# Kernel optimization log

Measured on AMD Instinct MI355X. Metric: run time of the kernel, lower is better.

The kernel has to match this reference:

```python
import jax, jax.numpy as jnp
import numpy as np

DIM = 384
H = W = 56
WS = 7
SS = 3
NH = 12
NMLP = 1536
N = WS * WS  # 49 tokens per window
EPS = 1e-5


def _rel_pos_index(ws):
    coords = np.stack(np.meshgrid(np.arange(ws), np.arange(ws), indexing='ij')).reshape(2, -1)
    rel = (coords[:, :, None] - coords[:, None, :]).transpose(1, 2, 0)
    rel[:, :, 0] += ws - 1
    rel[:, :, 1] += ws - 1
    rel[:, :, 0] *= 2 * ws - 1
    return rel.sum(-1)  # (N, N) int


def _attn_mask(Hh, Ww, ws, ss):
    img = np.zeros((Hh, Ww), dtype=np.float32)
    cnt = 0
    for h in (slice(0, -ws), slice(-ws, -ss), slice(-ss, None)):
        for w in (slice(0, -ws), slice(-ws, -ss), slice(-ss, None)):
            img[h, w] = cnt
            cnt += 1
    mw = img.reshape(Hh // ws, ws, Ww // ws, ws).transpose(0, 2, 1, 3).reshape(-1, ws * ws)
    diff = mw[:, None, :] - mw[:, :, None]  # (nW, N, N)
    return np.where(diff != 0, np.float32(-100.0), np.float32(0.0))


_REL_IDX = jnp.asarray(_rel_pos_index(WS))          # (49, 49)
_MASK = jnp.asarray(_attn_mask(H, W, WS, SS))       # (64, 49, 49)


def _ln(x, g, b):
    mu = jnp.mean(x, axis=-1, keepdims=True)
    var = jnp.mean(jnp.square(x - mu), axis=-1, keepdims=True)
    return (x - mu) * jax.lax.rsqrt(var + EPS) * g + b


def setup_inputs() -> dict:
    key = jax.random.key(0)
    ks = jax.random.split(key, 8)
    s = 0.02
    return {
        'x': jax.random.normal(ks[0], (32, H * W, DIM), dtype=jnp.float32),
        'g1': jnp.ones((DIM,), jnp.float32),
        'be1': jnp.zeros((DIM,), jnp.float32),
        'w_qkv': jax.random.normal(ks[1], (DIM, 3 * DIM), jnp.float32) * s,
        'b_qkv': jnp.zeros((3 * DIM,), jnp.float32),
        'rel_table': jax.random.normal(ks[2], ((2 * WS - 1) ** 2, NH), jnp.float32) * s,
        'w_proj': jax.random.normal(ks[3], (DIM, DIM), jnp.float32) * s,
        'b_proj': jnp.zeros((DIM,), jnp.float32),
        'g2': jnp.ones((DIM,), jnp.float32),
        'be2': jnp.zeros((DIM,), jnp.float32),
        'w1': jax.random.normal(ks[4], (DIM, NMLP), jnp.float32) * s,
        'b1': jnp.zeros((NMLP,), jnp.float32),
        'w2': jax.random.normal(ks[5], (NMLP, DIM), jnp.float32) * s,
        'b2': jnp.zeros((DIM,), jnp.float32),
    }


def reference(x, g1, be1, w_qkv, b_qkv, rel_table, w_proj, b_proj, g2, be2, w1, b1, w2, b2):
    B, L, C = x.shape
    hd = C // NH
    scale = hd ** -0.5

    shortcut = x
    h = _ln(x, g1, be1).reshape(B, H, W, C)
    h = jnp.roll(h, (-SS, -SS), axis=(1, 2))
    # window partition -> (B*nW, N, C)
    xw = h.reshape(B, H // WS, WS, W // WS, WS, C).transpose(0, 1, 3, 2, 4, 5).reshape(-1, N, C)
    B_ = xw.shape[0]

    qkv = (xw @ w_qkv + b_qkv).reshape(B_, N, 3, NH, hd).transpose(2, 0, 3, 1, 4)
    q, k, v = qkv[0], qkv[1], qkv[2]  # (B_, NH, N, hd)
    attn = jnp.einsum('whid,whjd->whij', q, k) * scale  # (B_, NH, N, N)

    bias = rel_table[_REL_IDX.reshape(-1)].reshape(N, N, NH).transpose(2, 0, 1)
    attn = attn + bias[None]

    nW = _MASK.shape[0]
    attn = attn.reshape(B_ // nW, nW, NH, N, N) + _MASK[None, :, None]
    attn = attn.reshape(B_, NH, N, N)
    attn = jax.nn.softmax(attn, axis=-1)

    out = jnp.einsum('whij,whjd->whid', attn, v).transpose(0, 2, 1, 3).reshape(B_, N, C)
    out = out @ w_proj + b_proj

    # window reverse -> (B, H, W, C)
    out = out.reshape(B, H // WS, W // WS, WS, WS, C).transpose(0, 1, 3, 2, 4, 5).reshape(B, H, W, C)
    out = jnp.roll(out, (SS, SS), axis=(1, 2)).reshape(B, L, C)

    x1 = out + shortcut
    m = _ln(x1, g2, be2)
    m = jax.nn.gelu(m @ w1 + b1, approximate=False) @ w2 + b2
    return m + x1
```

## Files before the change

kernel.cpp:

```cpp
#include <hip/hip_runtime.h>
#include <hip/hip_bf16.h>
#include <math.h>

typedef __attribute__((ext_vector_type(8))) short bf16x8;
typedef __attribute__((ext_vector_type(4))) short bf16x4;
typedef __attribute__((ext_vector_type(4))) float f32x4;
typedef __hip_bfloat16 bf16;

#define NH 12
#define HD 32
#define NPAD 64
#define NWIN 2048
#define NTOK 100352
#define HBLK (NPAD*HD)
#define WBLK (3*NH*HBLK)

typedef __attribute__((address_space(3))) const void cv3;

#define STR2(x) #x
#define DSR(dst, base, OFF)                                                  \
  asm volatile("ds_read_b128 %0, %1 offset:" STR2(OFF)                       \
               : "=v"(dst) : "v"(base))

__device__ inline float wave_sum(float v) {
#pragma unroll
  for (int off = 32; off; off >>= 1) v += __shfl_xor(v, off);
  return v;
}

__device__ inline void load_lds16(const bf16* g, bf16* l) {
  __builtin_amdgcn_global_load_lds((const __attribute__((address_space(1))) void*)g,
                                   (__attribute__((address_space(3))) void*)l, 16, 0, 0);
}

__device__ inline short bfbits(float f) {
  bf16 h = __float2bfloat16(f);
  return *(short*)&h;
}

__global__ __launch_bounds__(256) void cast_transpose(const float* __restrict__ in,
                                                      bf16* __restrict__ out, int K, int N) {
  int e = blockIdx.x * 256 + threadIdx.x;
  if (e >= K * N) return;
  int n = e / K, k = e - n * K;
  out[e] = __float2bfloat16(in[k * N + n]);
}

__global__ __launch_bounds__(256) void zero_pads(bf16* __restrict__ qkv) {
  int idx = blockIdx.x * 256 + threadIdx.x;
  const int total = NWIN * 3 * NH * 15 * HD;
  if (idx >= total) return;
  int d = idx & 31; int rest = idx >> 5;
  int n = 49 + (rest % 15); rest /= 15;
  int h = rest % NH; rest /= NH;
  int which = rest % 3; int w = rest / 3;
  size_t base = (size_t)w * WBLK + (size_t)which * NH * HBLK + (size_t)h * HBLK;
  size_t addr = (which == 2) ? base + (size_t)d * NPAD + n : base + (size_t)n * HD + d;
  qkv[addr] = __float2bfloat16(0.0f);
}

__global__ __launch_bounds__(256) void build_bias(const float* __restrict__ rel,
                                                  float* __restrict__ tbl) {
  int e = blockIdx.x * 256 + threadIdx.x;
  if (e >= 4 * 12 * 49 * 64) return;
  int col = e & 63; int t = e >> 6;
  int row = t % 49; t /= 49;
  int h = t % 12; int cls = t / 12;
  float v;
  if (col >= 49) {
    v = -1e30f;
  } else {
    int py = row / 7, px = row - py * 7;
    int qy = col / 7, qx = col - qy * 7;
    int ridx = (py - qy + 6) * 13 + (px - qx + 6);
    v = rel[ridx * 12 + h];
    int wy7 = cls >> 1, wx7 = cls & 1;
    int ly_r = wy7 ? (py < 4 ? 1 : 2) : 0;
    int lx_r = wx7 ? (px < 4 ? 1 : 2) : 0;
    int ly_c = wy7 ? (qy < 4 ? 1 : 2) : 0;
    int lx_c = wx7 ? (qx < 4 ? 1 : 2) : 0;
    if ((ly_r * 3 + lx_r) != (ly_c * 3 + lx_c)) v += -100.0f;
  }
  tbl[e] = v;
}

template <int MODE>
__global__ __launch_bounds__(256) void ln_kernel(const float* __restrict__ x,
                                                 const float* __restrict__ g,
                                                 const float* __restrict__ be,
                                                 bf16* __restrict__ out) {
  int wv = threadIdx.x >> 6, lane = threadIdx.x & 63;
  int t = blockIdx.x * 4 + wv;
  size_t src;
  if (MODE == 0) {
    int w = t / 49, n = t - w * 49;
    int b = w >> 6, wi = w & 63;
    int wy = wi >> 3, wx = wi & 7;
    int py = n / 7, px = n - py * 7;
    int rr = wy * 7 + py, cc = wx * 7 + px;
    int ro = rr + 3; if (ro >= 56) ro -= 56;
    int co = cc + 3; if (co >= 56) co -= 56;
    src = (size_t)b * 3136 + ro * 56 + co;
  } else {
    src = (size_t)t;
  }
  const float2* row2 = (const float2*)(x + src * 384);
  float2 v[3]; float s = 0.f;
#pragma unroll
  for (int j = 0; j < 3; ++j) { v[j] = row2[lane + 64 * j]; s += v[j].x + v[j].y; }
  s = wave_sum(s);
  float mu = s * (1.f / 384.f);
  float q = 0.f;
#pragma unroll
  for (int j = 0; j < 3; ++j) {
    float dx = v[j].x - mu, dy = v[j].y - mu;
    q += dx * dx + dy * dy;
  }
  q = wave_sum(q);
  float rs = rsqrtf(q * (1.f / 384.f) + 1e-5f);
  uint* o = (uint*)(out + (size_t)t * 384);
  const float2* g2 = (const float2*)g;
  const float2* b2 = (const float2*)be;
#pragma unroll
  for (int j = 0; j < 3; ++j) {
    int c2 = lane + 64 * j;
    float2 gg = g2[c2], bb = b2[c2];
    float ox = (v[j].x - mu) * rs * gg.x + bb.x;
    float oy = (v[j].y - mu) * rs * gg.y + bb.y;
    o[c2] = (uint)(unsigned short)bfbits(ox) | ((uint)(unsigned short)bfbits(oy) << 16);
  }
}

template <int EPI>
__global__ __launch_bounds__(512, 2) void gemm_bf16(const bf16* __restrict__ A,
                                                    const bf16* __restrict__ BT,
                                                    int K, int NCOL, int row0,
                                                    const float* __restrict__ bias,
                                                    const float* __restrict__ extra,
                                                    void* __restrict__ outp) {
  __shared__ __align__(16) bf16 As[3][256 * 64];
  __shared__ __align__(16) bf16 Bs[3][128 * 64];
  int tid = threadIdx.x;
  int lane = tid & 63, wv = tid >> 6;
  int wr = wv >> 1, wc = wv & 1;
  int lr = lane & 15, lg = lane >> 4;

  int nwg = gridDim.x;
  int bid = blockIdx.x;
  int xcd = bid & 7, li = bid >> 3;
  int qq = nwg >> 3, rr8 = nwg & 7;
  int start = xcd * qq + (xcd < rr8 ? xcd : rr8);
  int lin = start + li;
  int brow = lin / NCOL, bcol = lin - brow * NCOL;

  const bf16* Ab = A + (size_t)brow * 256 * K;
  const bf16* Bb = BT + (size_t)bcol * 128 * K;

  int srow = lane >> 3;
  int scol = ((lane & 7) * 8) ^ (srow << 3);
  const bf16* aS = Ab + (size_t)(wv * 32 + srow) * K + scol;
  const bf16* bS = Bb + (size_t)(wv * 16 + srow) * K + scol;

  f32x4 acc[4][4] = {};
  int nk = K >> 6;
  int xorm = (lr & 7) << 3;

#define STAGE(buf)                                                        \
  {                                                                       \
    _Pragma("unroll") for (int c = 0; c < 4; ++c)                         \
        load_lds16(aS + (size_t)c * 8 * K, &As[buf][wv * 2048 + c * 512]);\
    _Pragma("unroll") for (int c = 0; c < 2; ++c)                         \
        load_lds16(bS + (size_t)c * 8 * K, &Bs[buf][wv * 1024 + c * 512]);\
    aS += 64; bS += 64;                                                   \
  }

  STAGE(0);
  STAGE(1);
  asm volatile("s_waitcnt vmcnt(6)" ::: "memory");
  __builtin_amdgcn_s_barrier();

  for (int kk = 0; kk < nk; ++kk) {
    int cur = kk % 3;
    if (kk + 2 < nk) STAGE((kk + 2) % 3);
    int k0 = (lg * 8) ^ xorm;
    int k1 = (32 + lg * 8) ^ xorm;
    cv3* pA0 = (cv3*)&As[cur][(wr * 64 + lr) * 64 + k0];
    cv3* pB0 = (cv3*)&Bs[cur][(wc * 64 + lr) * 64 + k0];
    cv3* pA1 = (cv3*)&As[cur][(wr * 64 + lr) * 64 + k1];
    cv3* pB1 = (cv3*)&Bs[cur][(wc * 64 + lr) * 64 + k1];
    bf16x8 a0[4], b0[4], a1[4], b1[4];
    DSR(a0[0], pA0, 0); DSR(a0[1], pA0, 2048); DSR(a0[2], pA0, 4096); DSR(a0[3], pA0, 6144);
    DSR(b0[0], pB0, 0); DSR(b0[1], pB0, 2048); DSR(b0[2], pB0, 4096); DSR(b0[3], pB0, 6144);
    asm volatile("s_waitcnt lgkmcnt(0)" ::: "memory");
    __builtin_amdgcn_sched_barrier(0);
    DSR(a1[0], pA1, 0); DSR(a1[1], pA1, 2048); DSR(a1[2], pA1, 4096); DSR(a1[3], pA1, 6144);
    DSR(b1[0], pB1, 0); DSR(b1[1], pB1, 2048); DSR(b1[2], pB1, 4096); DSR(b1[3], pB1, 6144);
    __builtin_amdgcn_sched_barrier(0);
#pragma unroll
    for (int i = 0; i < 4; ++i)
#pragma unroll
      for (int j = 0; j < 4; ++j)
        acc[i][j] = __builtin_amdgcn_mfma_f32_16x16x32_bf16(b0[j], a0[i], acc[i][j], 0, 0, 0);
    asm volatile("s_waitcnt lgkmcnt(0)" ::: "memory");
    __builtin_amdgcn_sched_barrier(0);
#pragma unroll
    for (int i = 0; i < 4; ++i)
#pragma unroll
      for (int j = 0; j < 4; ++j)
        acc[i][j] = __builtin_amdgcn_mfma_f32_16x16x32_bf16(b1[j], a1[i], acc[i][j], 0, 0, 0);
    if (kk + 1 < nk) {
      if (kk + 2 < nk)
        asm volatile("s_waitcnt vmcnt(6)" ::: "memory");
      else
        asm volatile("s_waitcnt vmcnt(0)" ::: "memory");
      __builtin_amdgcn_s_barrier();
    }
  }
#undef STAGE

  float4 bias4[4];
#pragma unroll
  for (int j = 0; j < 4; ++j)
    bias4[j] = *(const float4*)(bias + bcol * 128 + wc * 64 + j * 16 + lg * 4);

#pragma unroll
  for (int i = 0; i < 4; ++i) {
    int lrow = brow * 256 + wr * 64 + i * 16 + lr;
    int grow = row0 + lrow;
    int w_ = 0, n_ = 0; size_t tok = 0;
    if (EPI == 0 || EPI == 1) {
      w_ = grow / 49; n_ = grow - w_ * 49;
      if (EPI == 1) {
        int b_ = w_ >> 6, wi = w_ & 63;
        int wy = wi >> 3, wx = wi & 7;
        int py = n_ / 7, px = n_ - py * 7;
        int r2 = wy * 7 + py, c2 = wx * 7 + px;
        int ro = r2 + 3; if (ro >= 56) ro -= 56;
        int co = c2 + 3; if (co >= 56) co -= 56;
        tok = (size_t)b_ * 3136 + ro * 56 + co;
      }
    }
#pragma unroll
    for (int j = 0; j < 4; ++j) {
      int col = bcol * 128 + wc * 64 + j * 16 + lg * 4;
      float v0 = acc[i][j][0] + bias4[j].x;
      float v1 = acc[i][j][1] + bias4[j].y;
      float v2 = acc[i][j][2] + bias4[j].z;
      float v3 = acc[i][j][3] + bias4[j].w;
      if (EPI == 0) {
        int which = (col >= 768) ? 2 : (col >= 384 ? 1 : 0);
        int cc = col - which * 384;
        int hh = cc >> 5, d0 = cc & 31;
        size_t base = (size_t)w_ * WBLK + (size_t)which * NH * HBLK + (size_t)hh * HBLK;
        if (which == 2) {
          bf16* vp = (bf16*)outp + base + (size_t)d0 * NPAD + n_;
          vp[0] = __float2bfloat16(v0);
          vp[NPAD] = __float2bfloat16(v1);
          vp[2 * NPAD] = __float2bfloat16(v2);
          vp[3 * NPAD] = __float2bfloat16(v3);
        } else {
          bf16x4 p = {bfbits(v0), bfbits(v1), bfbits(v2), bfbits(v3)};
          *(bf16x4*)((bf16*)outp + base + (size_t)n_ * HD + d0) = p;
        }
      } else if (EPI == 1) {
        size_t oidx = tok * 384 + col;
        float4 e = *(const float4*)(extra + oidx);
        float4 o = {v0 + e.x, v1 + e.y, v2 + e.z, v3 + e.w};
        *(float4*)((float*)outp + oidx) = o;
      } else if (EPI == 2) {
        float g0 = 0.5f * v0 * (1.0f + erff(v0 * 0.70710678118654752f));
        float g1 = 0.5f * v1 * (1.0f + erff(v1 * 0.70710678118654752f));
        float g2 = 0.5f * v2 * (1.0f + erff(v2 * 0.70710678118654752f));
        float g3 = 0.5f * v3 * (1.0f + erff(v3 * 0.70710678118654752f));
        bf16x4 p = {bfbits(g0), bfbits(g1), bfbits(g2), bfbits(g3)};
        *(bf16x4*)((bf16*)outp + (size_t)lrow * 1536 + col) = p;
      } else {
        size_t oidx = (size_t)grow * 384 + col;
        float4 e = *(const float4*)(extra + oidx);
        float4 o = {v0 + e.x, v1 + e.y, v2 + e.z, v3 + e.w};
        *(float4*)((float*)outp + oidx) = o;
      }
    }
  }
}

__global__ __launch_bounds__(256) void attn_kernel(const bf16* __restrict__ qkv,
                                                   const float* __restrict__ tbl,
                                                   bf16* __restrict__ attn_out) {
  __shared__ __align__(16) bf16 P[4][64 * 72];
  int wv = threadIdx.x >> 6, lane = threadIdx.x & 63;
  int lr = lane & 15, lg = lane >> 4;
  int w = blockIdx.x;
  int wi = w & 63, wy = wi >> 3, wx = wi & 7;
  int cls = ((wy == 7) ? 2 : 0) | ((wx == 7) ? 1 : 0);
  const bf16* base = qkv + (size_t)w * WBLK;
  bf16* Pl = &P[wv][0];
  const float scale = 0.17677669529663689f;

  for (int hh = 0; hh < 3; ++hh) {
    int h = wv + hh * 4;
    const bf16* Q  = base + (size_t)h * HBLK;
    const bf16* Kp = base + (size_t)(NH + h) * HBLK;
    const bf16* Vt = base + (size_t)(2 * NH + h) * HBLK;
    const float* tb = tbl + (size_t)(cls * 12 + h) * 49 * 64;

    bf16x8 qa[4], kb[4];
#pragma unroll
    for (int t = 0; t < 4; ++t) {
      qa[t] = *(const bf16x8*)(Q  + (t * 16 + lr) * 32 + lg * 8);
      kb[t] = *(const bf16x8*)(Kp + (t * 16 + lr) * 32 + lg * 8);
    }
    f32x4 S[4][4] = {};
#pragma unroll
    for (int i = 0; i < 4; ++i)
#pragma unroll
      for (int j = 0; j < 4; ++j)
        S[i][j] = __builtin_amdgcn_mfma_f32_16x16x32_bf16(qa[i], kb[j], S[i][j], 0, 0, 0);

#pragma unroll
    for (int i = 0; i < 4; ++i) {
#pragma unroll
      for (int r = 0; r < 4; ++r) {
        int row = i * 16 + lg * 4 + r;
        const float* trow = tb + (row < 49 ? row : 0) * 64;
        float sv[4]; float m = -1e30f;
#pragma unroll
        for (int j = 0; j < 4; ++j) {
          float s = S[i][j][r] * scale + trow[j * 16 + lr];
          sv[j] = s;
          m = fmaxf(m, s);
        }
        m = fmaxf(m, __shfl_xor(m, 1));
        m = fmaxf(m, __shfl_xor(m, 2));
        m = fmaxf(m, __shfl_xor(m, 4));
        m = fmaxf(m, __shfl_xor(m, 8));
        float ev[4]; float sum = 0.f;
#pragma unroll
        for (int j = 0; j < 4; ++j) { ev[j] = __expf(sv[j] - m); sum += ev[j]; }
        sum += __shfl_xor(sum, 1);
        sum += __shfl_xor(sum, 2);
        sum += __shfl_xor(sum, 4);
        sum += __shfl_xor(sum, 8);
        float inv = 1.0f / sum;
#pragma unroll
        for (int j = 0; j < 4; ++j)
          Pl[row * 72 + j * 16 + lr] = __float2bfloat16(ev[j] * inv);
      }
    }

    bf16x8 vb[2][2];
#pragma unroll
    for (int kt = 0; kt < 2; ++kt)
#pragma unroll
      for (int cj = 0; cj < 2; ++cj)
        vb[kt][cj] = *(const bf16x8*)(Vt + (cj * 16 + lr) * 64 + kt * 32 + lg * 8);
    f32x4 O[4][2] = {};
#pragma unroll
    for (int i = 0; i < 4; ++i) {
#pragma unroll
      for (int kt = 0; kt < 2; ++kt) {
        bf16x8 pa = *(const bf16x8*)(Pl + (i * 16 + lr) * 72 + kt * 32 + lg * 8);
#pragma unroll
        for (int cj = 0; cj < 2; ++cj)
          O[i][cj] = __builtin_amdgcn_mfma_f32_16x16x32_bf16(pa, vb[kt][cj], O[i][cj], 0, 0, 0);
      }
    }
#pragma unroll
    for (int i = 0; i < 4; ++i)
#pragma unroll
      for (int cj = 0; cj < 2; ++cj)
#pragma unroll
        for (int r = 0; r < 4; ++r) {
          int n = i * 16 + lg * 4 + r;
          if (n < 49)
            attn_out[((size_t)w * 49 + n) * 384 + h * 32 + cj * 16 + lr] =
                __float2bfloat16(O[i][cj][r]);
        }
  }
}

extern "C" void kernel_launch(void* const* d_in, const int* in_sizes, int n_in,
                              void* d_out, int out_size, void* d_ws, size_t ws_size,
                              hipStream_t stream) {
  (void)in_sizes; (void)n_in; (void)out_size;
  const float* x     = (const float*)d_in[0];
  const float* g1    = (const float*)d_in[1];
  const float* be1   = (const float*)d_in[2];
  const float* w_qkv = (const float*)d_in[3];
  const float* b_qkv = (const float*)d_in[4];
  const float* rel   = (const float*)d_in[5];
  const float* w_pr  = (const float*)d_in[6];
  const float* b_pr  = (const float*)d_in[7];
  const float* g2    = (const float*)d_in[8];
  const float* be2   = (const float*)d_in[9];
  const float* w1    = (const float*)d_in[10];
  const float* b1    = (const float*)d_in[11];
  const float* w2    = (const float*)d_in[12];
  const float* b2    = (const float*)d_in[13];
  float* out = (float*)d_out;

  if (ws_size < 390070272u) return;

  char* ws = (char*)d_ws;
  bf16* wqkvT = (bf16*)(ws);
  bf16* wprT  = (bf16*)(ws + 884736);
  bf16* w1T   = (bf16*)(ws + 1179648);
  bf16* w2T   = (bf16*)(ws + 2359296);
  float* btbl = (float*)(ws + 3538944);
  bf16* xw    = (bf16*)(ws + (4u << 20));
  bf16* qkv   = (bf16*)(ws + (84u << 20));
  bf16* m_in  = qkv;
  bf16* h1    = (bf16*)(ws + (164u << 20));

  cast_transpose<<<dim3((442368 + 255) / 256), 256, 0, stream>>>(w_qkv, wqkvT, 384, 1152);
  cast_transpose<<<dim3((147456 + 255) / 256), 256, 0, stream>>>(w_pr, wprT, 384, 384);
  cast_transpose<<<dim3((589824 + 255) / 256), 256, 0, stream>>>(w1, w1T, 384, 1536);
  cast_transpose<<<dim3((589824 + 255) / 256), 256, 0, stream>>>(w2, w2T, 1536, 384);

  build_bias<<<dim3((4 * 12 * 49 * 64 + 255) / 256), 256, 0, stream>>>(rel, btbl);

  zero_pads<<<dim3((NWIN * 3 * NH * 15 * HD + 255) / 256), 256, 0, stream>>>(qkv);

  ln_kernel<0><<<dim3(NTOK / 4), 256, 0, stream>>>(x, g1, be1, xw);

  gemm_bf16<0><<<dim3(3528), 512, 0, stream>>>(xw, wqkvT, 384, 9, 0, b_qkv, nullptr, (void*)qkv);

  attn_kernel<<<dim3(NWIN), 256, 0, stream>>>(qkv, btbl, xw);

  gemm_bf16<1><<<dim3(1176), 512, 0, stream>>>(xw, wprT, 384, 3, 0, b_pr, x, (void*)out);

  ln_kernel<1><<<dim3(NTOK / 4), 256, 0, stream>>>(out, g2, be2, m_in);

  for (int c = 0; c < 2; ++c) {
    gemm_bf16<2><<<dim3(2352), 512, 0, stream>>>(m_in + (size_t)c * 50176 * 384, w1T, 384,
                                                 12, c * 50176, b1, nullptr, (void*)h1);
    gemm_bf16<3><<<dim3(588), 512, 0, stream>>>(h1, w2T, 1536, 3, c * 50176, b2, out,
                                                (void*)out);
  }
}
```

Before: 982.8 us.

## Enlarge GEMM row tile to 512 with K-step 32 and MFMA priority hints

```diff
diff --git a/kernel.cpp b/kernel.cpp
--- a/kernel.cpp
+++ b/kernel.cpp
@@ -138,8 +138,8 @@
                                                     const float* __restrict__ bias,
                                                     const float* __restrict__ extra,
                                                     void* __restrict__ outp) {
-  __shared__ __align__(16) bf16 As[3][256 * 64];
-  __shared__ __align__(16) bf16 Bs[3][128 * 64];
+  __shared__ __align__(16) bf16 As[3][512 * 32];
+  __shared__ __align__(16) bf16 Bs[3][128 * 32];
   int tid = threadIdx.x;
   int lane = tid & 63, wv = tid >> 6;
   int wr = wv >> 1, wc = wv & 1;
@@ -153,64 +153,61 @@
   int lin = start + li;
   int brow = lin / NCOL, bcol = lin - brow * NCOL;
 
-  const bf16* Ab = A + (size_t)brow * 256 * K;
+  const bf16* Ab = A + (size_t)brow * 512 * K;
   const bf16* Bb = BT + (size_t)bcol * 128 * K;
 
-  int srow = lane >> 3;
-  int scol = ((lane & 7) * 8) ^ (srow << 3);
-  const bf16* aS = Ab + (size_t)(wv * 32 + srow) * K + scol;
+  int srow = lane >> 2;
+  int scol = ((lane & 3) ^ ((srow >> 1) & 3)) * 8;
+  const bf16* aS = Ab + (size_t)(wv * 64 + srow) * K + scol;
   const bf16* bS = Bb + (size_t)(wv * 16 + srow) * K + scol;
 
-  f32x4 acc[4][4] = {};
-  int nk = K >> 6;
-  int xorm = (lr & 7) << 3;
-
-#define STAGE(buf)                                                        \
-  {                                                                       \
-    _Pragma("unroll") for (int c = 0; c < 4; ++c)                         \
-        load_lds16(aS + (size_t)c * 8 * K, &As[buf][wv * 2048 + c * 512]);\
-    _Pragma("unroll") for (int c = 0; c < 2; ++c)                         \
-        load_lds16(bS + (size_t)c * 8 * K, &Bs[buf][wv * 1024 + c * 512]);\
-    aS += 64; bS += 64;                                                   \
+  f32x4 acc[8][4] = {};
+  int nk = K >> 5;
+  int koff = (lg * 8) ^ (((lr >> 1) & 3) * 8);
+
+#define STAGE(buf)                                                            \
+  {                                                                           \
+    _Pragma("unroll") for (int c = 0; c < 4; ++c)                             \
+        load_lds16(aS + (size_t)c * 16 * K, &As[buf][wv * 2048 + c * 512]);   \
+    load_lds16(bS, &Bs[buf][wv * 512]);                                       \
+    aS += 32; bS += 32;                                                       \
   }
 
   STAGE(0);
   STAGE(1);
-  asm volatile("s_waitcnt vmcnt(6)" ::: "memory");
+  asm volatile("s_waitcnt vmcnt(5)" ::: "memory");
   __builtin_amdgcn_s_barrier();
 
   for (int kk = 0; kk < nk; ++kk) {
     int cur = kk % 3;
     if (kk + 2 < nk) STAGE((kk + 2) % 3);
-    int k0 = (lg * 8) ^ xorm;
-    int k1 = (32 + lg * 8) ^ xorm;
-    cv3* pA0 = (cv3*)&As[cur][(wr * 64 + lr) * 64 + k0];
-    cv3* pB0 = (cv3*)&Bs[cur][(wc * 64 + lr) * 64 + k0];
-    cv3* pA1 = (cv3*)&As[cur][(wr * 64 + lr) * 64 + k1];
-    cv3* pB1 = (cv3*)&Bs[cur][(wc * 64 + lr) * 64 + k1];
-    bf16x8 a0[4], b0[4], a1[4], b1[4];
-    DSR(a0[0], pA0, 0); DSR(a0[1], pA0, 2048); DSR(a0[2], pA0, 4096); DSR(a0[3], pA0, 6144);
-    DSR(b0[0], pB0, 0); DSR(b0[1], pB0, 2048); DSR(b0[2], pB0, 4096); DSR(b0[3], pB0, 6144);
+    cv3* pA = (cv3*)&As[cur][(wr * 128 + lr) * 32 + koff];
+    cv3* pB = (cv3*)&Bs[cur][(wc * 64 + lr) * 32 + koff];
+    bf16x8 a[8], b[4];
+    DSR(a[0], pA, 0); DSR(a[1], pA, 1024); DSR(a[2], pA, 2048); DSR(a[3], pA, 3072);
+    DSR(b[0], pB, 0); DSR(b[1], pB, 1024); DSR(b[2], pB, 2048); DSR(b[3], pB, 3072);
+    DSR(a[4], pA, 4096); DSR(a[5], pA, 5120); DSR(a[6], pA, 6144); DSR(a[7], pA, 7168);
+    asm volatile("s_waitcnt lgkmcnt(4)" ::: "memory");
+    __builtin_amdgcn_sched_barrier(0);
+    __builtin_amdgcn_s_setprio(1);
+#pragma unroll
+    for (int i = 0; i < 4; ++i)
+#pragma unroll
+      for (int j = 0; j < 4; ++j)
+        acc[i][j] = __builtin_amdgcn_mfma_f32_16x16x32_bf16(b[j], a[i], acc[i][j], 0, 0, 0);
+    __builtin_amdgcn_s_setprio(0);
     asm volatile("s_waitcnt lgkmcnt(0)" ::: "memory");
     __builtin_amdgcn_sched_barrier(0);
-    DSR(a1[0], pA1, 0); DSR(a1[1], pA1, 2048); DSR(a1[2], pA1, 4096); DSR(a1[3], pA1, 6144);
-    DSR(b1[0], pB1, 0); DSR(b1[1], pB1, 2048); DSR(b1[2], pB1, 4096); DSR(b1[3], pB1, 6144);
-    __builtin_amdgcn_sched_barrier(0);
-#pragma unroll
-    for (int i = 0; i < 4; ++i)
+    __builtin_amdgcn_s_setprio(1);
+#pragma unroll
+    for (int i = 4; i < 8; ++i)
 #pragma unroll
       for (int j = 0; j < 4; ++j)
-        acc[i][j] = __builtin_amdgcn_mfma_f32_16x16x32_bf16(b0[j], a0[i], acc[i][j], 0, 0, 0);
-    asm volatile("s_waitcnt lgkmcnt(0)" ::: "memory");
-    __builtin_amdgcn_sched_barrier(0);
-#pragma unroll
-    for (int i = 0; i < 4; ++i)
-#pragma unroll
-      for (int j = 0; j < 4; ++j)
-        acc[i][j] = __builtin_amdgcn_mfma_f32_16x16x32_bf16(b1[j], a1[i], acc[i][j], 0, 0, 0);
+        acc[i][j] = __builtin_amdgcn_mfma_f32_16x16x32_bf16(b[j], a[i], acc[i][j], 0, 0, 0);
+    __builtin_amdgcn_s_setprio(0);
     if (kk + 1 < nk) {
       if (kk + 2 < nk)
-        asm volatile("s_waitcnt vmcnt(6)" ::: "memory");
+        asm volatile("s_waitcnt vmcnt(5)" ::: "memory");
       else
         asm volatile("s_waitcnt vmcnt(0)" ::: "memory");
       __builtin_amdgcn_s_barrier();
@@ -224,8 +221,8 @@
     bias4[j] = *(const float4*)(bias + bcol * 128 + wc * 64 + j * 16 + lg * 4);
 
 #pragma unroll
-  for (int i = 0; i < 4; ++i) {
-    int lrow = brow * 256 + wr * 64 + i * 16 + lr;
+  for (int i = 0; i < 8; ++i) {
+    int lrow = brow * 512 + wr * 128 + i * 16 + lr;
     int grow = row0 + lrow;
     int w_ = 0, n_ = 0; size_t tok = 0;
     if (EPI == 0 || EPI == 1) {
@@ -423,18 +420,18 @@
 
   ln_kernel<0><<<dim3(NTOK / 4), 256, 0, stream>>>(x, g1, be1, xw);
 
-  gemm_bf16<0><<<dim3(3528), 512, 0, stream>>>(xw, wqkvT, 384, 9, 0, b_qkv, nullptr, (void*)qkv);
+  gemm_bf16<0><<<dim3(1764), 512, 0, stream>>>(xw, wqkvT, 384, 9, 0, b_qkv, nullptr, (void*)qkv);
 
   attn_kernel<<<dim3(NWIN), 256, 0, stream>>>(qkv, btbl, xw);
 
-  gemm_bf16<1><<<dim3(1176), 512, 0, stream>>>(xw, wprT, 384, 3, 0, b_pr, x, (void*)out);
+  gemm_bf16<1><<<dim3(588), 512, 0, stream>>>(xw, wprT, 384, 3, 0, b_pr, x, (void*)out);
 
   ln_kernel<1><<<dim3(NTOK / 4), 256, 0, stream>>>(out, g2, be2, m_in);
 
   for (int c = 0; c < 2; ++c) {
-    gemm_bf16<2><<<dim3(2352), 512, 0, stream>>>(m_in + (size_t)c * 50176 * 384, w1T, 384,
+    gemm_bf16<2><<<dim3(1176), 512, 0, stream>>>(m_in + (size_t)c * 50176 * 384, w1T, 384,
                                                  12, c * 50176, b1, nullptr, (void*)h1);
-    gemm_bf16<3><<<dim3(588), 512, 0, stream>>>(h1, w2T, 1536, 3, c * 50176, b2, out,
+    gemm_bf16<3><<<dim3(294), 512, 0, stream>>>(h1, w2T, 1536, 3, c * 50176, b2, out,
                                                 (void*)out);
   }
 }
```

New measurement: 1.105 ms. 1.12x slower.

## Interleave split global prefetch with MFMA phases using barriers and setprio

Applied to the files above, without the earlier changes.

```diff
diff --git a/kernel.cpp b/kernel.cpp
--- a/kernel.cpp
+++ b/kernel.cpp
@@ -173,6 +173,19 @@
         load_lds16(bS + (size_t)c * 8 * K, &Bs[buf][wv * 1024 + c * 512]);\
     aS += 64; bS += 64;                                                   \
   }
+#define STAGE_H0(buf)                                                     \
+  {                                                                       \
+    load_lds16(aS, &As[buf][wv * 2048]);                                  \
+    load_lds16(aS + (size_t)8 * K, &As[buf][wv * 2048 + 512]);            \
+    load_lds16(bS, &Bs[buf][wv * 1024]);                                  \
+  }
+#define STAGE_H1(buf)                                                     \
+  {                                                                       \
+    load_lds16(aS + (size_t)16 * K, &As[buf][wv * 2048 + 1024]);          \
+    load_lds16(aS + (size_t)24 * K, &As[buf][wv * 2048 + 1536]);          \
+    load_lds16(bS + (size_t)8 * K, &Bs[buf][wv * 1024 + 512]);            \
+    aS += 64; bS += 64;                                                   \
+  }
 
   STAGE(0);
   STAGE(1);
@@ -181,7 +194,8 @@
 
   for (int kk = 0; kk < nk; ++kk) {
     int cur = kk % 3;
-    if (kk + 2 < nk) STAGE((kk + 2) % 3);
+    int nxt = (kk + 2) % 3;
+    bool pf = (kk + 2 < nk);
     int k0 = (lg * 8) ^ xorm;
     int k1 = (32 + lg * 8) ^ xorm;
     cv3* pA0 = (cv3*)&As[cur][(wr * 64 + lr) * 64 + k0];
@@ -189,27 +203,37 @@
     cv3* pA1 = (cv3*)&As[cur][(wr * 64 + lr) * 64 + k1];
     cv3* pB1 = (cv3*)&Bs[cur][(wc * 64 + lr) * 64 + k1];
     bf16x8 a0[4], b0[4], a1[4], b1[4];
+
     DSR(a0[0], pA0, 0); DSR(a0[1], pA0, 2048); DSR(a0[2], pA0, 4096); DSR(a0[3], pA0, 6144);
     DSR(b0[0], pB0, 0); DSR(b0[1], pB0, 2048); DSR(b0[2], pB0, 4096); DSR(b0[3], pB0, 6144);
+    if (pf) STAGE_H0(nxt);
+    __builtin_amdgcn_s_barrier();
     asm volatile("s_waitcnt lgkmcnt(0)" ::: "memory");
     __builtin_amdgcn_sched_barrier(0);
+    __builtin_amdgcn_s_setprio(1);
+#pragma unroll
+    for (int i = 0; i < 4; ++i)
+#pragma unroll
+      for (int j = 0; j < 4; ++j)
+        acc[i][j] = __builtin_amdgcn_mfma_f32_16x16x32_bf16(b0[j], a0[i], acc[i][j], 0, 0, 0);
+    __builtin_amdgcn_s_setprio(0);
+    __builtin_amdgcn_s_barrier();
+
     DSR(a1[0], pA1, 0); DSR(a1[1], pA1, 2048); DSR(a1[2], pA1, 4096); DSR(a1[3], pA1, 6144);
     DSR(b1[0], pB1, 0); DSR(b1[1], pB1, 2048); DSR(b1[2], pB1, 4096); DSR(b1[3], pB1, 6144);
-    __builtin_amdgcn_sched_barrier(0);
-#pragma unroll
-    for (int i = 0; i < 4; ++i)
-#pragma unroll
-      for (int j = 0; j < 4; ++j)
-        acc[i][j] = __builtin_amdgcn_mfma_f32_16x16x32_bf16(b0[j], a0[i], acc[i][j], 0, 0, 0);
+    if (pf) STAGE_H1(nxt);
+    __builtin_amdgcn_s_barrier();
     asm volatile("s_waitcnt lgkmcnt(0)" ::: "memory");
     __builtin_amdgcn_sched_barrier(0);
+    __builtin_amdgcn_s_setprio(1);
 #pragma unroll
     for (int i = 0; i < 4; ++i)
 #pragma unroll
       for (int j = 0; j < 4; ++j)
         acc[i][j] = __builtin_amdgcn_mfma_f32_16x16x32_bf16(b1[j], a1[i], acc[i][j], 0, 0, 0);
+    __builtin_amdgcn_s_setprio(0);
     if (kk + 1 < nk) {
-      if (kk + 2 < nk)
+      if (pf)
         asm volatile("s_waitcnt vmcnt(6)" ::: "memory");
       else
         asm volatile("s_waitcnt vmcnt(0)" ::: "memory");
@@ -217,6 +241,8 @@
     }
   }
 #undef STAGE
+#undef STAGE_H0
+#undef STAGE_H1
 
   float4 bias4[4];
 #pragma unroll
```

After: 1.001 ms. About the same (+1.9%).

## Fuse QKV projection into windowed attention kernel, removing qkv intermediate buffer

Applied to the files above, without the earlier changes.

```diff
diff --git a/kernel.cpp b/kernel.cpp
--- a/kernel.cpp
+++ b/kernel.cpp
@@ -9,11 +9,8 @@
 
 #define NH 12
 #define HD 32
-#define NPAD 64
 #define NWIN 2048
 #define NTOK 100352
-#define HBLK (NPAD*HD)
-#define WBLK (3*NH*HBLK)
 
 typedef __attribute__((address_space(3))) const void cv3;
 
@@ -44,19 +41,6 @@
   if (e >= K * N) return;
   int n = e / K, k = e - n * K;
   out[e] = __float2bfloat16(in[k * N + n]);
-}
-
-__global__ __launch_bounds__(256) void zero_pads(bf16* __restrict__ qkv) {
-  int idx = blockIdx.x * 256 + threadIdx.x;
-  const int total = NWIN * 3 * NH * 15 * HD;
-  if (idx >= total) return;
-  int d = idx & 31; int rest = idx >> 5;
-  int n = 49 + (rest % 15); rest /= 15;
-  int h = rest % NH; rest /= NH;
-  int which = rest % 3; int w = rest / 3;
-  size_t base = (size_t)w * WBLK + (size_t)which * NH * HBLK + (size_t)h * HBLK;
-  size_t addr = (which == 2) ? base + (size_t)d * NPAD + n : base + (size_t)n * HD + d;
-  qkv[addr] = __float2bfloat16(0.0f);
 }
 
 __global__ __launch_bounds__(256) void build_bias(const float* __restrict__ rel,
@@ -227,18 +211,16 @@
   for (int i = 0; i < 4; ++i) {
     int lrow = brow * 256 + wr * 64 + i * 16 + lr;
     int grow = row0 + lrow;
-    int w_ = 0, n_ = 0; size_t tok = 0;
-    if (EPI == 0 || EPI == 1) {
-      w_ = grow / 49; n_ = grow - w_ * 49;
-      if (EPI == 1) {
-        int b_ = w_ >> 6, wi = w_ & 63;
-        int wy = wi >> 3, wx = wi & 7;
-        int py = n_ / 7, px = n_ - py * 7;
-        int r2 = wy * 7 + py, c2 = wx * 7 + px;
-        int ro = r2 + 3; if (ro >= 56) ro -= 56;
-        int co = c2 + 3; if (co >= 56) co -= 56;
-        tok = (size_t)b_ * 3136 + ro * 56 + co;
-      }
+    size_t tok = 0;
+    if (EPI == 1) {
+      int w_ = grow / 49, n_ = grow - (grow / 49) * 49;
+      int b_ = w_ >> 6, wi = w_ & 63;
+      int wy = wi >> 3, wx = wi & 7;
+      int py = n_ / 7, px = n_ - py * 7;
+      int r2 = wy * 7 + py, c2 = wx * 7 + px;
+      int ro = r2 + 3; if (ro >= 56) ro -= 56;
+      int co = c2 + 3; if (co >= 56) co -= 56;
+      tok = (size_t)b_ * 3136 + ro * 56 + co;
     }
 #pragma unroll
     for (int j = 0; j < 4; ++j) {
@@ -247,22 +229,7 @@
       float v1 = acc[i][j][1] + bias4[j].y;
       float v2 = acc[i][j][2] + bias4[j].z;
       float v3 = acc[i][j][3] + bias4[j].w;
-      if (EPI == 0) {
-        int which = (col >= 768) ? 2 : (col >= 384 ? 1 : 0);
-        int cc = col - which * 384;
-        int hh = cc >> 5, d0 = cc & 31;
-        size_t base = (size_t)w_ * WBLK + (size_t)which * NH * HBLK + (size_t)hh * HBLK;
-        if (which == 2) {
-          bf16* vp = (bf16*)outp + base + (size_t)d0 * NPAD + n_;
-          vp[0] = __float2bfloat16(v0);
-          vp[NPAD] = __float2bfloat16(v1);
-          vp[2 * NPAD] = __float2bfloat16(v2);
-          vp[3 * NPAD] = __float2bfloat16(v3);
-        } else {
-          bf16x4 p = {bfbits(v0), bfbits(v1), bfbits(v2), bfbits(v3)};
-          *(bf16x4*)((bf16*)outp + base + (size_t)n_ * HD + d0) = p;
-        }
-      } else if (EPI == 1) {
+      if (EPI == 1) {
         size_t oidx = tok * 384 + col;
         float4 e = *(const float4*)(extra + oidx);
         float4 o = {v0 + e.x, v1 + e.y, v2 + e.z, v3 + e.w};
@@ -284,31 +251,77 @@
   }
 }
 
-__global__ __launch_bounds__(256) void attn_kernel(const bf16* __restrict__ qkv,
-                                                   const float* __restrict__ tbl,
-                                                   bf16* __restrict__ attn_out) {
-  __shared__ __align__(16) bf16 P[4][64 * 72];
-  int wv = threadIdx.x >> 6, lane = threadIdx.x & 63;
+__global__ __launch_bounds__(256) void fused_qkv_attn(bf16* __restrict__ xw,
+                                                      const bf16* __restrict__ wT,
+                                                      const float* __restrict__ bqkv,
+                                                      const float* __restrict__ tbl) {
+  __shared__ __align__(16) bf16 At[64 * 384];
+  __shared__ __align__(16) bf16 Scr[4][7424];
+  int tid = threadIdx.x;
+  int lane = tid & 63, wv = tid >> 6;
   int lr = lane & 15, lg = lane >> 4;
   int w = blockIdx.x;
   int wi = w & 63, wy = wi >> 3, wx = wi & 7;
   int cls = ((wy == 7) ? 2 : 0) | ((wx == 7) ? 1 : 0);
-  const bf16* base = qkv + (size_t)w * WBLK;
-  bf16* Pl = &P[wv][0];
   const float scale = 0.17677669529663689f;
+
+  bf16* xrow = xw + (size_t)w * 49 * 384;
+  for (int idx = tid; idx < 64 * 48; idx += 256) {
+    int r = idx / 48, g = idx - r * 48;
+    bf16x8 v = {};
+    if (r < 49) v = *(const bf16x8*)(xrow + r * 384 + g * 8);
+    *(bf16x8*)(&At[r * 384 + ((g ^ (r & 7)) << 3)]) = v;
+  }
+  __syncthreads();
+
+  bf16* Q  = &Scr[wv][0];
+  bf16* Kl = &Scr[wv][2560];
+  bf16* Vt = &Scr[wv][5120];
+  bf16* Pl = &Scr[wv][0];
+
+  int axor = (lr & 7) << 3;
 
   for (int hh = 0; hh < 3; ++hh) {
     int h = wv + hh * 4;
-    const bf16* Q  = base + (size_t)h * HBLK;
-    const bf16* Kp = base + (size_t)(NH + h) * HBLK;
-    const bf16* Vt = base + (size_t)(2 * NH + h) * HBLK;
-    const float* tb = tbl + (size_t)(cls * 12 + h) * 49 * 64;
+#pragma unroll
+    for (int mat = 0; mat < 3; ++mat) {
+      int cb = mat * 384 + h * 32;
+      const bf16* wb = wT + (size_t)(cb + lr) * 384 + lg * 8;
+      f32x4 acc[4][2] = {};
+#pragma unroll
+      for (int kk = 0; kk < 12; ++kk) {
+        int k0 = kk * 32;
+        bf16x8 b0 = *(const bf16x8*)(wb + k0);
+        bf16x8 b1 = *(const bf16x8*)(wb + 16 * 384 + k0);
+        int ko = (k0 + lg * 8) ^ axor;
+#pragma unroll
+        for (int m = 0; m < 4; ++m) {
+          bf16x8 a = *(const bf16x8*)(&At[(m * 16 + lr) * 384 + ko]);
+          acc[m][0] = __builtin_amdgcn_mfma_f32_16x16x32_bf16(a, b0, acc[m][0], 0, 0, 0);
+          acc[m][1] = __builtin_amdgcn_mfma_f32_16x16x32_bf16(a, b1, acc[m][1], 0, 0, 0);
+        }
+      }
+      float bia0 = bqkv[cb + lr], bia1 = bqkv[cb + 16 + lr];
+#pragma unroll
+      for (int m = 0; m < 4; ++m)
+#pragma unroll
+        for (int n = 0; n < 2; ++n)
+#pragma unroll
+          for (int r = 0; r < 4; ++r) {
+            int row = m * 16 + lg * 4 + r;
+            int col = n * 16 + lr;
+            float v = acc[m][n][r] + (n ? bia1 : bia0);
+            if (mat == 2) Vt[col * 72 + row] = __float2bfloat16(v);
+            else if (mat == 0) Q[row * 40 + col] = __float2bfloat16(v);
+            else Kl[row * 40 + col] = __float2bfloat16(v);
+          }
+    }
 
     bf16x8 qa[4], kb[4];
 #pragma unroll
     for (int t = 0; t < 4; ++t) {
-      qa[t] = *(const bf16x8*)(Q  + (t * 16 + lr) * 32 + lg * 8);
-      kb[t] = *(const bf16x8*)(Kp + (t * 16 + lr) * 32 + lg * 8);
+      qa[t] = *(const bf16x8*)(&Q[(t * 16 + lr) * 40 + lg * 8]);
+      kb[t] = *(const bf16x8*)(&Kl[(t * 16 + lr) * 40 + lg * 8]);
     }
     f32x4 S[4][4] = {};
 #pragma unroll
@@ -317,6 +330,7 @@
       for (int j = 0; j < 4; ++j)
         S[i][j] = __builtin_amdgcn_mfma_f32_16x16x32_bf16(qa[i], kb[j], S[i][j], 0, 0, 0);
 
+    const float* tb = tbl + (size_t)(cls * 12 + h) * 49 * 64;
 #pragma unroll
     for (int i = 0; i < 4; ++i) {
 #pragma unroll
@@ -353,13 +367,13 @@
     for (int kt = 0; kt < 2; ++kt)
 #pragma unroll
       for (int cj = 0; cj < 2; ++cj)
-        vb[kt][cj] = *(const bf16x8*)(Vt + (cj * 16 + lr) * 64 + kt * 32 + lg * 8);
+        vb[kt][cj] = *(const bf16x8*)(&Vt[(cj * 16 + lr) * 72 + kt * 32 + lg * 8]);
     f32x4 O[4][2] = {};
 #pragma unroll
     for (int i = 0; i < 4; ++i) {
 #pragma unroll
       for (int kt = 0; kt < 2; ++kt) {
-        bf16x8 pa = *(const bf16x8*)(Pl + (i * 16 + lr) * 72 + kt * 32 + lg * 8);
+        bf16x8 pa = *(const bf16x8*)(&Pl[(i * 16 + lr) * 72 + kt * 32 + lg * 8]);
 #pragma unroll
         for (int cj = 0; cj < 2; ++cj)
           O[i][cj] = __builtin_amdgcn_mfma_f32_16x16x32_bf16(pa, vb[kt][cj], O[i][cj], 0, 0, 0);
@@ -373,7 +387,7 @@
         for (int r = 0; r < 4; ++r) {
           int n = i * 16 + lg * 4 + r;
           if (n < 49)
-            attn_out[((size_t)w * 49 + n) * 384 + h * 32 + cj * 16 + lr] =
+            xw[((size_t)w * 49 + n) * 384 + h * 32 + cj * 16 + lr] =
                 __float2bfloat16(O[i][cj][r]);
         }
   }
@@ -408,8 +422,7 @@
   bf16* w2T   = (bf16*)(ws + 2359296);
   float* btbl = (float*)(ws + 3538944);
   bf16* xw    = (bf16*)(ws + (4u << 20));
-  bf16* qkv   = (bf16*)(ws + (84u << 20));
-  bf16* m_in  = qkv;
+  bf16* m_in  = (bf16*)(ws + (84u << 20));
   bf16* h1    = (bf16*)(ws + (164u << 20));
 
   cast_transpose<<<dim3((442368 + 255) / 256), 256, 0, stream>>>(w_qkv, wqkvT, 384, 1152);
@@ -419,13 +432,9 @@
 
   build_bias<<<dim3((4 * 12 * 49 * 64 + 255) / 256), 256, 0, stream>>>(rel, btbl);
 
-  zero_pads<<<dim3((NWIN * 3 * NH * 15 * HD + 255) / 256), 256, 0, stream>>>(qkv);
-
   ln_kernel<0><<<dim3(NTOK / 4), 256, 0, stream>>>(x, g1, be1, xw);
 
-  gemm_bf16<0><<<dim3(3528), 512, 0, stream>>>(xw, wqkvT, 384, 9, 0, b_qkv, nullptr, (void*)qkv);
-
-  attn_kernel<<<dim3(NWIN), 256, 0, stream>>>(qkv, btbl, xw);
+  fused_qkv_attn<<<dim3(NWIN), 256, 0, stream>>>(xw, wqkvT, b_qkv, btbl);
 
   gemm_bf16<1><<<dim3(1176), 512, 0, stream>>>(xw, wprT, 384, 3, 0, b_pr, x, (void*)out);
 
```

Measured after the change: 1.041 ms. 5.9% more time.
